# Kernel tuning notes

Measured on AMD Instinct MI355X. Metric: run time of the kernel, lower is better.

The kernel has to match this reference:

```python
import jax, jax.numpy as jnp
import numpy as np

N_USERS = 40000
N_POIS = 20000
D = 128
N_EDGES = 500000
N_LAYERS = 2
B = 256
NPOS = 100
TOPK = 20


def setup_inputs() -> dict:
    key = jax.random.key(0)
    ks = jax.random.split(key, 24)
    # guarantee every user row / poi col has at least one edge (avoids 0-norm rows)
    er = jnp.concatenate([jnp.arange(N_USERS, dtype=jnp.int32),
                          jax.random.randint(ks[0], (N_EDGES - N_USERS,), 0, N_USERS, jnp.int32)])
    ec = jnp.concatenate([jnp.arange(N_USERS, dtype=jnp.int32) % N_POIS,
                          jax.random.randint(ks[1], (N_EDGES - N_USERS,), 0, N_POIS, jnp.int32)])
    w0 = lambda k, shape: jax.random.normal(k, shape, jnp.float32) * 0.05
    return {
        'edge_row': er,
        'edge_col': ec,
        'click_vals': jax.random.uniform(ks[2], (N_EDGES,), jnp.float32),
        'favor_vals': jax.random.uniform(ks[3], (N_EDGES,), jnp.float32),
        'consume_vals': jax.random.uniform(ks[4], (N_EDGES,), jnp.float32),
        'uid_embed': w0(ks[5], (N_USERS, D)),
        'pid_embed': w0(ks[6], (N_POIS, D)),
        'user_index': jax.random.randint(ks[7], (B, 1), 0, N_USERS, jnp.int32),
        'poi_index': jax.random.randint(ks[8], (B, NPOS), 0, N_POIS, jnp.int32),
        'labels': (jax.random.uniform(ks[9], (B, NPOS)) < 0.5).astype(jnp.float32),
        'global_user_feature': w0(ks[10], (N_USERS, D)),
        'w': w0(ks[11], (1, 3)),
        'fw': w0(ks[12], (3, 1)),
        'W_user_click': w0(ks[13], (D, D)),
        'W_poi_click': w0(ks[14], (D, D)),
        'W_user_favor': w0(ks[15], (D, D)),
        'W_poi_favor': w0(ks[16], (D, D)),
        'W_user_consume': w0(ks[17], (D, D)),
        'W_poi_consume': w0(ks[18], (D, D)),
        'Ws': w0(ks[19], (D, D)),
        'bs_bias': w0(ks[20], (D,)),
    }


def reference(edge_row, edge_col, click_vals, favor_vals, consume_vals, uid_embed, pid_embed,
              user_index, poi_index, labels, global_user_feature, w, fw,
              W_user_click, W_poi_click, W_user_favor, W_poi_favor,
              W_user_consume, W_poi_consume, Ws, bs_bias):
    n_users, n_pois = uid_embed.shape[0], pid_embed.shape[0]
    batch_user = user_index.reshape(-1)

    def gcn(vals, Wu, Wp):
        # bipartite GCN propagation: A @ p (user side), A.T @ u (poi side)
        su, sp = uid_embed, pid_embed          # running sums of per-layer normalized features
        u, p = uid_embed, pid_embed            # un-normalized propagated features
        for _ in range(N_LAYERS):
            u = jax.ops.segment_sum(vals[:, None] * p[edge_col], edge_row, num_segments=n_users)
            su = su + u / jnp.linalg.norm(u, axis=1, keepdims=True)
            p = jax.ops.segment_sum(vals[:, None] * u[edge_row], edge_col, num_segments=n_pois)
            sp = sp + p / jnp.linalg.norm(p, axis=1, keepdims=True)
        uf = su @ Wu.T                         # final_user_linear (bias=False)
        pf = sp @ Wp.T                         # final_poi_linear (bias=False)
        return uf[batch_user] @ pf.T, uf       # [B, n_pois], [n_users, D]

    wn = jax.nn.softmax(w, axis=1)
    fwn = jax.nn.softmax(fw, axis=0)

    click_up, click_uf = gcn(click_vals, W_user_click, W_poi_click)
    favor_up, favor_uf = gcn(favor_vals + 1e-18 * click_vals, W_user_favor, W_poi_favor)
    consume_up, consume_uf = gcn(consume_vals + 1e-18 * click_vals, W_user_consume, W_poi_consume)

    alt = favor_up * wn[0, 0] + click_up * wn[0, 1] + consume_up * wn[0, 2]
    predict = jnp.take_along_axis(alt, poi_index, axis=1)                      # [B, NPOS]
    # BCEWithLogitsLoss (mean reduction), numerically stable form
    select_loss = jnp.mean(jax.nn.relu(predict) - predict * labels + jnp.log1p(jnp.exp(-jnp.abs(predict))))

    L = user_index.shape[1]
    cur = batch_user[jnp.arange(0, user_index.shape[0] * L, L)]                # first user of each row
    # gcn_user_feature stacked (favor, consume, click) @ fw
    id_feat = favor_uf * fwn[0, 0] + consume_uf * fwn[1, 0] + click_uf * fwn[2, 0]

    # Select_Layer (all inputs to matmuls are detached in the original)
    id_d = jax.lax.stop_gradient(id_feat)
    bs = id_d[cur] @ Ws.T + bs_bias
    uu = bs @ id_d.T                                                           # [B, n_users]
    top_score, top_idx = jax.lax.top_k(uu, TOPK)
    top_score = jax.nn.softmax(jax.lax.stop_gradient(top_score), axis=-1)
    neigh = jax.lax.stop_gradient(global_user_feature[top_idx])                # [B, TOPK, D]
    user_feature = jnp.einsum('bk,bkd->bd', top_score, neigh)
    return select_loss, user_feature
```

## Files before the change

### kernel.cpp

```cpp
#include <hip/hip_runtime.h>

#define N_USERS 40000
#define N_POIS  20000
#define DIM     128
#define N_EDGES 500000
#define BATCH   256
#define NPOS    100
#define TOPK    20
#define NCHUNK  128
#define CPT     313
#define SCHUNK  1024
#define RCH     40
#define CCH     20
#define LOSS_BLOCKS 25

typedef _Float16 f16x8 __attribute__((ext_vector_type(8)));
typedef float f32x4 __attribute__((ext_vector_type(4)));

__device__ __forceinline__ int iclamp(int x, int lo, int hi) {
    return x < lo ? lo : (x > hi ? hi : x);
}
__device__ __forceinline__ float2 h2f2(unsigned int u) {
    union { unsigned int u32; _Float16 h[2]; } v; v.u32 = u;
    return make_float2((float)v.h[0], (float)v.h[1]);
// ... 205 lines not shown
__global__ __launch_bounds__(256) void spmm_kernel(
        const int* __restrict__ ptr, const int4* __restrict__ pack,
        const unsigned short* __restrict__ src,
        unsigned short* __restrict__ raw_h,
        const float* __restrict__ base,
        float* __restrict__ acc, int nrows) {
    int wid = (blockIdx.x * blockDim.x + threadIdx.x) >> 6;
    int lane = threadIdx.x & 63;
    if (wid >= nrows) return;
    int beg = __builtin_amdgcn_readfirstlane(iclamp(ptr[wid], 0, N_EDGES));
    int end = __builtin_amdgcn_readfirstlane(iclamp(ptr[wid + 1], 0, N_EDGES));
    if (end < beg) end = beg;
    float ax = 0.f, ay = 0.f;
    int e = beg;
    int lo2 = lane * 2;
    for (; e + 8 <= end; e += 8) {
        int4 q0 = pack[e + 0], q1 = pack[e + 1], q2 = pack[e + 2], q3 = pack[e + 3];
        int4 q4 = pack[e + 4], q5 = pack[e + 5], q6 = pack[e + 6], q7 = pack[e + 7];
        float v0 = pickvT<CH>(q0), v1 = pickvT<CH>(q1), v2 = pickvT<CH>(q2), v3 = pickvT<CH>(q3);
        float v4 = pickvT<CH>(q4), v5 = pickvT<CH>(q5), v6 = pickvT<CH>(q6), v7 = pickvT<CH>(q7);
        float2 p0 = h2f2(*(const unsigned int*)(src + (size_t)q0.x * DIM + lo2));
        float2 p1 = h2f2(*(const unsigned int*)(src + (size_t)q1.x * DIM + lo2));
        float2 p2 = h2f2(*(const unsigned int*)(src + (size_t)q2.x * DIM + lo2));
        float2 p3 = h2f2(*(const unsigned int*)(src + (size_t)q3.x * DIM + lo2));
        float2 p4 = h2f2(*(const unsigned int*)(src + (size_t)q4.x * DIM + lo2));
        float2 p5 = h2f2(*(const unsigned int*)(src + (size_t)q5.x * DIM + lo2));
        float2 p6 = h2f2(*(const unsigned int*)(src + (size_t)q6.x * DIM + lo2));
        float2 p7 = h2f2(*(const unsigned int*)(src + (size_t)q7.x * DIM + lo2));
        ax = fmaf(v0, p0.x, fmaf(v1, p1.x, fmaf(v2, p2.x, fmaf(v3, p3.x, ax))));
        ax = fmaf(v4, p4.x, fmaf(v5, p5.x, fmaf(v6, p6.x, fmaf(v7, p7.x, ax))));
        ay = fmaf(v0, p0.y, fmaf(v1, p1.y, fmaf(v2, p2.y, fmaf(v3, p3.y, ay))));
        ay = fmaf(v4, p4.y, fmaf(v5, p5.y, fmaf(v6, p6.y, fmaf(v7, p7.y, ay))));
    }
    if (e < end) {
        int last = end - 1;
        int e1 = e + 1 <= last ? e + 1 : last;
        int e2 = e + 2 <= last ? e + 2 : last;
        int e3 = e + 3 <= last ? e + 3 : last;
        int e4 = e + 4 <= last ? e + 4 : last;
        int e5 = e + 5 <= last ? e + 5 : last;
        int e6 = e + 6 <= last ? e + 6 : last;
        int e7 = e + 7 <= last ? e + 7 : last;
        int4 q0 = pack[e], q1 = pack[e1], q2 = pack[e2], q3 = pack[e3];
        int4 q4 = pack[e4], q5 = pack[e5], q6 = pack[e6], q7 = pack[e7];
        float v0 = pickvT<CH>(q0);
        float v1 = (e + 1 < end) ? pickvT<CH>(q1) : 0.f;
        float v2 = (e + 2 < end) ? pickvT<CH>(q2) : 0.f;
        float v3 = (e + 3 < end) ? pickvT<CH>(q3) : 0.f;
        float v4 = (e + 4 < end) ? pickvT<CH>(q4) : 0.f;
        float v5 = (e + 5 < end) ? pickvT<CH>(q5) : 0.f;
        float v6 = (e + 6 < end) ? pickvT<CH>(q6) : 0.f;
        float v7 = (e + 7 < end) ? pickvT<CH>(q7) : 0.f;
        float2 p0 = h2f2(*(const unsigned int*)(src + (size_t)q0.x * DIM + lo2));
        float2 p1 = h2f2(*(const unsigned int*)(src + (size_t)q1.x * DIM + lo2));
        float2 p2 = h2f2(*(const unsigned int*)(src + (size_t)q2.x * DIM + lo2));
        float2 p3 = h2f2(*(const unsigned int*)(src + (size_t)q3.x * DIM + lo2));
        float2 p4 = h2f2(*(const unsigned int*)(src + (size_t)q4.x * DIM + lo2));
        float2 p5 = h2f2(*(const unsigned int*)(src + (size_t)q5.x * DIM + lo2));
        float2 p6 = h2f2(*(const unsigned int*)(src + (size_t)q6.x * DIM + lo2));
        float2 p7 = h2f2(*(const unsigned int*)(src + (size_t)q7.x * DIM + lo2));
        ax = fmaf(v0, p0.x, fmaf(v1, p1.x, fmaf(v2, p2.x, fmaf(v3, p3.x, ax))));
        ax = fmaf(v4, p4.x, fmaf(v5, p5.x, fmaf(v6, p6.x, fmaf(v7, p7.x, ax))));
        ay = fmaf(v0, p0.y, fmaf(v1, p1.y, fmaf(v2, p2.y, fmaf(v3, p3.y, ay))));
        ay = fmaf(v4, p4.y, fmaf(v5, p5.y, fmaf(v6, p6.y, fmaf(v7, p7.y, ay))));
    }
    float n2 = ax * ax + ay * ay;
    #pragma unroll
    for (int o = 32; o > 0; o >>= 1) n2 += __shfl_xor(n2, o, 64);
    float inv = rsqrtf(fmaxf(n2, 1e-30f));
    *(unsigned int*)(raw_h + (size_t)wid * DIM + lo2) = f2h2(ax, ay);
    float2 bv = *(const float2*)(base + (size_t)wid * DIM + lo2);
    *(float2*)(acc + (size_t)wid * DIM + lo2) =
        make_float2(bv.x + ax * inv, bv.y + ay * inv);
}

__global__ __launch_bounds__(256) void spmm3_kernel(
        const int* __restrict__ ptr, const int4* __restrict__ pack,
        const unsigned short* __restrict__ src,
        unsigned short* __restrict__ r0, unsigned short* __restrict__ r1,
        unsigned short* __restrict__ r2, int nrows) {
    int wid = (blockIdx.x * blockDim.x + threadIdx.x) >> 6;
    int lane = threadIdx.x & 63;
    if (wid >= nrows) return;
    int beg = __builtin_amdgcn_readfirstlane(iclamp(ptr[wid], 0, N_EDGES));
    int end = __builtin_amdgcn_readfirstlane(iclamp(ptr[wid + 1], 0, N_EDGES));
    if (end < beg) end = beg;
    float a0x = 0.f, a0y = 0.f, a1x = 0.f, a1y = 0.f, a2x = 0.f, a2y = 0.f;
    int e = beg;
    int lo2 = lane * 2;
    for (; e + 4 <= end; e += 4) {
        int4 q0 = pack[e + 0], q1 = pack[e + 1], q2 = pack[e + 2], q3 = pack[e + 3];
        float2 p0 = h2f2(*(const unsigned int*)(src + (size_t)q0.x * DIM + lo2));
        float2 p1 = h2f2(*(const unsigned int*)(src + (size_t)q1.x * DIM + lo2));
        float2 p2 = h2f2(*(const unsigned int*)(src + (size_t)q2.x * DIM + lo2));
        float2 p3 = h2f2(*(const unsigned int*)(src + (size_t)q3.x * DIM + lo2));
        a0x = fmaf(__int_as_float(q0.y), p0.x, fmaf(__int_as_float(q1.y), p1.x,
              fmaf(__int_as_float(q2.y), p2.x, fmaf(__int_as_float(q3.y), p3.x, a0x))));
// ... 244 lines not shown
    float k0 = x0.x * x0.x + x0.y * x0.y;
    float k1 = x1.x * x1.x + x1.y * x1.y;
    float k2 = x2.x * x2.x + x2.y * x2.y;
    #pragma unroll
    for (int oo = 32; oo > 0; oo >>= 1) {
        m0 += __shfl_xor(m0, oo, 64); m1 += __shfl_xor(m1, oo, 64); m2 += __shfl_xor(m2, oo, 64);
        k0 += __shfl_xor(k0, oo, 64); k1 += __shfl_xor(k1, oo, 64); k2 += __shfl_xor(k2, oo, 64);
    }
    float im0 = rsqrtf(fmaxf(m0, 1e-30f)), ik0 = rsqrtf(fmaxf(k0, 1e-30f));
    float im1 = rsqrtf(fmaxf(m1, 1e-30f)), ik1 = rsqrtf(fmaxf(k1, 1e-30f));
    float im2 = rsqrtf(fmaxf(m2, 1e-30f)), ik2 = rsqrtf(fmaxf(k2, 1e-30f));
    float2 bv = *(const float2*)(pid + o);
    *(float2*)(sp0 + o) = make_float2(bv.x + x0.x * ik0 + a0x * im0, bv.y + x0.y * ik0 + a0y * im0);
    *(float2*)(sp1 + o) = make_float2(bv.x + x1.x * ik1 + a1x * im1, bv.y + x1.y * ik1 + a1y * im1);
    *(float2*)(sp2 + o) = make_float2(bv.x + x2.x * ik2 + a2x * im2, bv.y + x2.y * ik2 + a2y * im2);
}

template<int CH>
__global__ __launch_bounds__(256) void spmm_l2u_kernel(
        const int* __restrict__ ptr, const int4* __restrict__ pack,
        const unsigned short* __restrict__ src,
        unsigned short* __restrict__ u1raw,
        const float* __restrict__ uid,
        float* __restrict__ su, int nrows) {
    int wid = (blockIdx.x * blockDim.x + threadIdx.x) >> 6;
    int lane = threadIdx.x & 63;
    if (wid >= nrows) return;
    int beg = __builtin_amdgcn_readfirstlane(iclamp(ptr[wid], 0, N_EDGES));
    int end = __builtin_amdgcn_readfirstlane(iclamp(ptr[wid + 1], 0, N_EDGES));
    if (end < beg) end = beg;
    float ax = 0.f, ay = 0.f;
    int e = beg;
    int lo2 = lane * 2;
    for (; e + 8 <= end; e += 8) {
        int4 q0 = pack[e + 0], q1 = pack[e + 1], q2 = pack[e + 2], q3 = pack[e + 3];
        int4 q4 = pack[e + 4], q5 = pack[e + 5], q6 = pack[e + 6], q7 = pack[e + 7];
        float v0 = pickvT<CH>(q0), v1 = pickvT<CH>(q1), v2 = pickvT<CH>(q2), v3 = pickvT<CH>(q3);
        float v4 = pickvT<CH>(q4), v5 = pickvT<CH>(q5), v6 = pickvT<CH>(q6), v7 = pickvT<CH>(q7);
        float2 p0 = h2f2(*(const unsigned int*)(src + (size_t)q0.x * DIM + lo2));
        float2 p1 = h2f2(*(const unsigned int*)(src + (size_t)q1.x * DIM + lo2));
        float2 p2 = h2f2(*(const unsigned int*)(src + (size_t)q2.x * DIM + lo2));
        float2 p3 = h2f2(*(const unsigned int*)(src + (size_t)q3.x * DIM + lo2));
        float2 p4 = h2f2(*(const unsigned int*)(src + (size_t)q4.x * DIM + lo2));
        float2 p5 = h2f2(*(const unsigned int*)(src + (size_t)q5.x * DIM + lo2));
        float2 p6 = h2f2(*(const unsigned int*)(src + (size_t)q6.x * DIM + lo2));
        float2 p7 = h2f2(*(const unsigned int*)(src + (size_t)q7.x * DIM + lo2));
        ax = fmaf(v0, p0.x, fmaf(v1, p1.x, fmaf(v2, p2.x, fmaf(v3, p3.x, ax))));
        ax = fmaf(v4, p4.x, fmaf(v5, p5.x, fmaf(v6, p6.x, fmaf(v7, p7.x, ax))));
        ay = fmaf(v0, p0.y, fmaf(v1, p1.y, fmaf(v2, p2.y, fmaf(v3, p3.y, ay))));
        ay = fmaf(v4, p4.y, fmaf(v5, p5.y, fmaf(v6, p6.y, fmaf(v7, p7.y, ay))));
    }
    if (e < end) {
        int last = end - 1;
        int e1 = e + 1 <= last ? e + 1 : last;
        int e2 = e + 2 <= last ? e + 2 : last;
        int e3 = e + 3 <= last ? e + 3 : last;
        int e4 = e + 4 <= last ? e + 4 : last;
        int e5 = e + 5 <= last ? e + 5 : last;
        int e6 = e + 6 <= last ? e + 6 : last;
        int e7 = e + 7 <= last ? e + 7 : last;
        int4 q0 = pack[e], q1 = pack[e1], q2 = pack[e2], q3 = pack[e3];
        int4 q4 = pack[e4], q5 = pack[e5], q6 = pack[e6], q7 = pack[e7];
        float v0 = pickvT<CH>(q0);
        float v1 = (e + 1 < end) ? pickvT<CH>(q1) : 0.f;
        float v2 = (e + 2 < end) ? pickvT<CH>(q2) : 0.f;
        float v3 = (e + 3 < end) ? pickvT<CH>(q3) : 0.f;
        float v4 = (e + 4 < end) ? pickvT<CH>(q4) : 0.f;
        float v5 = (e + 5 < end) ? pickvT<CH>(q5) : 0.f;
        float v6 = (e + 6 < end) ? pickvT<CH>(q6) : 0.f;
        float v7 = (e + 7 < end) ? pickvT<CH>(q7) : 0.f;
        float2 p0 = h2f2(*(const unsigned int*)(src + (size_t)q0.x * DIM + lo2));
        float2 p1 = h2f2(*(const unsigned int*)(src + (size_t)q1.x * DIM + lo2));
        float2 p2 = h2f2(*(const unsigned int*)(src + (size_t)q2.x * DIM + lo2));
        float2 p3 = h2f2(*(const unsigned int*)(src + (size_t)q3.x * DIM + lo2));
        float2 p4 = h2f2(*(const unsigned int*)(src + (size_t)q4.x * DIM + lo2));
        float2 p5 = h2f2(*(const unsigned int*)(src + (size_t)q5.x * DIM + lo2));
        float2 p6 = h2f2(*(const unsigned int*)(src + (size_t)q6.x * DIM + lo2));
        float2 p7 = h2f2(*(const unsigned int*)(src + (size_t)q7.x * DIM + lo2));
        ax = fmaf(v0, p0.x, fmaf(v1, p1.x, fmaf(v2, p2.x, fmaf(v3, p3.x, ax))));
        ax = fmaf(v4, p4.x, fmaf(v5, p5.x, fmaf(v6, p6.x, fmaf(v7, p7.x, ax))));
        ay = fmaf(v0, p0.y, fmaf(v1, p1.y, fmaf(v2, p2.y, fmaf(v3, p3.y, ay))));
        ay = fmaf(v4, p4.y, fmaf(v5, p5.y, fmaf(v6, p6.y, fmaf(v7, p7.y, ay))));
    }
    size_t o = (size_t)wid * DIM + lo2;
    float2 u1 = h2f2(*(const unsigned int*)(u1raw + o));
    float n2a = ax * ax + ay * ay;
    float n2b = u1.x * u1.x + u1.y * u1.y;
    #pragma unroll
    for (int oo = 32; oo > 0; oo >>= 1) {
        n2a += __shfl_xor(n2a, oo, 64);
        n2b += __shfl_xor(n2b, oo, 64);
    }
    float i2 = rsqrtf(fmaxf(n2a, 1e-30f));
    float i1 = rsqrtf(fmaxf(n2b, 1e-30f));
    *(unsigned int*)(u1raw + o) = f2h2(ax, ay);
    float2 bv = *(const float2*)(uid + o);
    *(float2*)(su + o) = make_float2(bv.x + u1.x * i1 + ax * i2,
                                     bv.y + u1.y * i1 + ay * i2);
}

template<int CH>
__global__ __launch_bounds__(256) void spmm_l2p_kernel(
        const int* __restrict__ ptr, const int4* __restrict__ pack,
        const unsigned short* __restrict__ src,
        const unsigned short* __restrict__ p1raw,
        const float* __restrict__ pid,
        float* __restrict__ sp, int nrows) {
    int wid = (blockIdx.x * blockDim.x + threadIdx.x) >> 6;
    int lane = threadIdx.x & 63;
    if (wid >= nrows) return;
    int beg = __builtin_amdgcn_readfirstlane(iclamp(ptr[wid], 0, N_EDGES));
    int end = __builtin_amdgcn_readfirstlane(iclamp(ptr[wid + 1], 0, N_EDGES));
    if (end < beg) end = beg;
    float ax = 0.f, ay = 0.f;
    int e = beg;
    int lo2 = lane * 2;
    for (; e + 8 <= end; e += 8) {
        int4 q0 = pack[e + 0], q1 = pack[e + 1], q2 = pack[e + 2], q3 = pack[e + 3];
        int4 q4 = pack[e + 4], q5 = pack[e + 5], q6 = pack[e + 6], q7 = pack[e + 7];
        float v0 = pickvT<CH>(q0), v1 = pickvT<CH>(q1), v2 = pickvT<CH>(q2), v3 = pickvT<CH>(q3);
        float v4 = pickvT<CH>(q4), v5 = pickvT<CH>(q5), v6 = pickvT<CH>(q6), v7 = pickvT<CH>(q7);
        float2 p0 = h2f2(*(const unsigned int*)(src + (size_t)q0.x * DIM + lo2));
        float2 p1 = h2f2(*(const unsigned int*)(src + (size_t)q1.x * DIM + lo2));
        float2 p2 = h2f2(*(const unsigned int*)(src + (size_t)q2.x * DIM + lo2));
        float2 p3 = h2f2(*(const unsigned int*)(src + (size_t)q3.x * DIM + lo2));
        float2 p4 = h2f2(*(const unsigned int*)(src + (size_t)q4.x * DIM + lo2));
        float2 p5 = h2f2(*(const unsigned int*)(src + (size_t)q5.x * DIM + lo2));
        float2 p6 = h2f2(*(const unsigned int*)(src + (size_t)q6.x * DIM + lo2));
        float2 p7 = h2f2(*(const unsigned int*)(src + (size_t)q7.x * DIM + lo2));
        ax = fmaf(v0, p0.x, fmaf(v1, p1.x, fmaf(v2, p2.x, fmaf(v3, p3.x, ax))));
        ax = fmaf(v4, p4.x, fmaf(v5, p5.x, fmaf(v6, p6.x, fmaf(v7, p7.x, ax))));
        ay = fmaf(v0, p0.y, fmaf(v1, p1.y, fmaf(v2, p2.y, fmaf(v3, p3.y, ay))));
        ay = fmaf(v4, p4.y, fmaf(v5, p5.y, fmaf(v6, p6.y, fmaf(v7, p7.y, ay))));
    }
    if (e < end) {
        int last = end - 1;
        int e1 = e + 1 <= last ? e + 1 : last;
        int e2 = e + 2 <= last ? e + 2 : last;
        int e3 = e + 3 <= last ? e + 3 : last;
        int e4 = e + 4 <= last ? e + 4 : last;
        int e5 = e + 5 <= last ? e + 5 : last;
        int e6 = e + 6 <= last ? e + 6 : last;
        int e7 = e + 7 <= last ? e + 7 : last;
        int4 q0 = pack[e], q1 = pack[e1], q2 = pack[e2], q3 = pack[e3];
        int4 q4 = pack[e4], q5 = pack[e5], q6 = pack[e6], q7 = pack[e7];
        float v0 = pickvT<CH>(q0);
        float v1 = (e + 1 < end) ? pickvT<CH>(q1) : 0.f;
        float v2 = (e + 2 < end) ? pickvT<CH>(q2) : 0.f;
        float v3 = (e + 3 < end) ? pickvT<CH>(q3) : 0.f;
        float v4 = (e + 4 < end) ? pickvT<CH>(q4) : 0.f;
        float v5 = (e + 5 < end) ? pickvT<CH>(q5) : 0.f;
        float v6 = (e + 6 < end) ? pickvT<CH>(q6) : 0.f;
        float v7 = (e + 7 < end) ? pickvT<CH>(q7) : 0.f;
        float2 p0 = h2f2(*(const unsigned int*)(src + (size_t)q0.x * DIM + lo2));
        float2 p1 = h2f2(*(const unsigned int*)(src + (size_t)q1.x * DIM + lo2));
        float2 p2 = h2f2(*(const unsigned int*)(src + (size_t)q2.x * DIM + lo2));
        float2 p3 = h2f2(*(const unsigned int*)(src + (size_t)q3.x * DIM + lo2));
        float2 p4 = h2f2(*(const unsigned int*)(src + (size_t)q4.x * DIM + lo2));
        float2 p5 = h2f2(*(const unsigned int*)(src + (size_t)q5.x * DIM + lo2));
        float2 p6 = h2f2(*(const unsigned int*)(src + (size_t)q6.x * DIM + lo2));
        float2 p7 = h2f2(*(const unsigned int*)(src + (size_t)q7.x * DIM + lo2));
        ax = fmaf(v0, p0.x, fmaf(v1, p1.x, fmaf(v2, p2.x, fmaf(v3, p3.x, ax))));
        ax = fmaf(v4, p4.x, fmaf(v5, p5.x, fmaf(v6, p6.x, fmaf(v7, p7.x, ax))));
        ay = fmaf(v0, p0.y, fmaf(v1, p1.y, fmaf(v2, p2.y, fmaf(v3, p3.y, ay))));
        ay = fmaf(v4, p4.y, fmaf(v5, p5.y, fmaf(v6, p6.y, fmaf(v7, p7.y, ay))));
    }
    size_t o = (size_t)wid * DIM + lo2;
    float2 p1v = h2f2(*(const unsigned int*)(p1raw + o));
    float n2a = ax * ax + ay * ay;
    float n2b = p1v.x * p1v.x + p1v.y * p1v.y;
    #pragma unroll
    for (int oo = 32; oo > 0; oo >>= 1) {
        n2a += __shfl_xor(n2a, oo, 64);
        n2b += __shfl_xor(n2b, oo, 64);
    }
    float i2 = rsqrtf(fmaxf(n2a, 1e-30f));
    float i1 = rsqrtf(fmaxf(n2b, 1e-30f));
    float2 bv = *(const float2*)(pid + o);
    *(float2*)(sp + o) = make_float2(bv.x + p1v.x * i1 + ax * i2,
                                     bv.y + p1v.y * i1 + ay * i2);
}

__global__ __launch_bounds__(256) void gemm_mfma_kernel(
        const float* __restrict__ A, const float* __restrict__ W,
        float* __restrict__ store, float* __restrict__ accum,
        _Float16* __restrict__ accum_h,
        const float* __restrict__ fw3, int fsel, int first, int M) {
    int w = threadIdx.x >> 6, l = threadIdx.x & 63;
    int lg = l >> 4, lc = l & 15;
    int j0 = w * 32;
    float coef = accum ? softmax3(fw3, fsel) : 0.f;
    f16x8 Bf[2][4];
    #pragma unroll
    for (int t = 0; t < 2; t++) {
        const float* wr = W + (size_t)(j0 + t * 16 + lc) * DIM + lg * 8;
        #pragma unroll
        for (int s = 0; s < 4; s++) Bf[t][s] = frag8(wr + s * 32);
    }
// ... 7 lines not shown
        #pragma unroll
        for (int s = 0; s < 4; s++) Af[s] = frag8(arow + s * 32);
        f32x4 acc0 = {0.f, 0.f, 0.f, 0.f};
        f32x4 acc1 = {0.f, 0.f, 0.f, 0.f};
        #pragma unroll
        for (int s = 0; s < 4; s++) {
            acc0 = __builtin_amdgcn_mfma_f32_16x16x32_f16(Af[s], Bf[0][s], acc0, 0, 0, 0);
            acc1 = __builtin_amdgcn_mfma_f32_16x16x32_f16(Af[s], Bf[1][s], acc1, 0, 0, 0);
        }
        int rbase = u0 + lg * 4;
        #pragma unroll
        for (int r = 0; r < 4; r++) {
            int row = rbase + r;
            if (row >= M) continue;
            size_t o0 = (size_t)row * DIM + j0 + lc;
            size_t o1 = o0 + 16;
            if (store) { store[o0] = acc0[r]; store[o1] = acc1[r]; }
            if (accum) {
                float p0 = first ? 0.f : accum[o0];
                float p1 = first ? 0.f : accum[o1];
                float n0 = p0 + coef * acc0[r];
                float n1 = p1 + coef * acc1[r];
                accum[o0] = n0;
                accum[o1] = n1;
                if (accum_h) {
                    accum_h[o0] = (_Float16)n0;
                    accum_h[o1] = (_Float16)n1;
                }
            }
        }
    }
}

__global__ void ufsel_kernel(const float* __restrict__ su, const float* __restrict__ W,
                             const int* __restrict__ uidx, float* __restrict__ outsel) {
    int b = blockIdx.x, j = threadIdx.x;
    __shared__ float ar[128];
    int u = iclamp(uidx[b], 0, N_USERS - 1);
    ar[j] = su[(size_t)u * DIM + j];
    __syncthreads();
    const float4* Wr = (const float4*)(W + (size_t)j * DIM);
    float acc = 0.f;
    #pragma unroll 8
    for (int q = 0; q < 32; q++) {
        float4 wq = Wr[q];
        acc = fmaf(ar[4 * q + 0], wq.x, acc);
        acc = fmaf(ar[4 * q + 1], wq.y, acc);
        acc = fmaf(ar[4 * q + 2], wq.z, acc);
        acc = fmaf(ar[4 * q + 3], wq.w, acc);
    }
    outsel[(size_t)b * DIM + j] = acc;
}

__global__ __launch_bounds__(256) void predict_kernel(
        const float* __restrict__ ufs, const float* __restrict__ pf,
        const int* __restrict__ pidx, const float* __restrict__ w3,
        int wsel, int first, float* __restrict__ alt) {
    int wid = (blockIdx.x * blockDim.x + threadIdx.x) >> 6;
    int lane = threadIdx.x & 63;
    if (wid >= BATCH * NPOS) return;
    int b = wid / NPOS;
    int poi = iclamp(pidx[wid], 0, N_POIS - 1);
    const float2 uv = *(const float2*)(ufs + (size_t)b * DIM + lane * 2);
    const float2 pv = *(const float2*)(pf + (size_t)poi * DIM + lane * 2);
    float s = uv.x * pv.x + uv.y * pv.y;
    #pragma unroll
    for (int o = 32; o > 0; o >>= 1) s += __shfl_xor(s, o, 64);
    if (lane == 0) {
        float coef = softmax3(w3, wsel);
        float prev = first ? 0.f : alt[wid];
        alt[wid] = prev + coef * s;
    }
}

__global__ void loss_part_kernel(const float* __restrict__ alt, const float* __restrict__ labels,
                                 float* __restrict__ part) {
    int b = blockIdx.x, t = threadIdx.x;
    int i = b * 1024 + t * 4;
    float4 x4 = *(const float4*)(alt + i);
    float4 y4 = *(const float4*)(labels + i);
    float s = 0.f;
    s += fmaxf(x4.x, 0.f) - x4.x * y4.x + log1pf(expf(-fabsf(x4.x)));
    s += fmaxf(x4.y, 0.f) - x4.y * y4.y + log1pf(expf(-fabsf(x4.y)));
    s += fmaxf(x4.z, 0.f) - x4.z * y4.z + log1pf(expf(-fabsf(x4.z)));
// ... 227 lines not shown
    int* rcnt = cnts;
    int* ccnt = cnts + N_USERS;
    int* scanws = (int*)carve(4 * 2 * (RCH + CCH) + 4 * 64);
    int* rsum = scanws;
    int* csum = rsum + RCH;
    int* rbase = csum + CCH;
    int* cbase = rbase + RCH;
    float* losspart = (float*)carve(4 * (LOSS_BLOCKS + 7));
    int4* rpack = (int4*)carve(16ll * N_EDGES);
    int4* cpack = (int4*)carve(16ll * N_EDGES);
    unsigned short* pid_h = (unsigned short*)carve(2ll * N_POIS * DIM);
    unsigned short* utr0 = (unsigned short*)carve(2ll * N_USERS * DIM);
    unsigned short* ptr_h = (unsigned short*)carve(2ll * N_POIS * DIM);
    float* su  = (float*)carve(4ll * N_USERS * DIM);
    float* sp  = (float*)carve(4ll * N_POIS * DIM);
    float* idf = (float*)carve(4ll * N_USERS * DIM);
    float* pf = (float*)utr0;
    float* cand_s = su;
    int*   cand_i = (int*)(su + (size_t)NCHUNK * BATCH * TOPK);
    _Float16* idf_h = (_Float16*)rpack;
    _Float16* bst_h = (_Float16*)bst;
    int* rord = (int*)su;
    int* cord = rord + N_EDGES;
    unsigned short* utr1 = (unsigned short*)carve(2ll * N_USERS * DIM);
    unsigned short* utr2 = (unsigned short*)carve(2ll * N_USERS * DIM);
    unsigned short* p1b1 = (unsigned short*)carve(2ll * N_POIS * DIM);
    unsigned short* p1b2 = (unsigned short*)carve(2ll * N_POIS * DIM);
    bool fused = (off <= ws_size);
    float* su1 = (float*)carve(4ll * N_USERS * DIM);
    float* su2 = (float*)carve(4ll * N_USERS * DIM);
    float* sp1 = (float*)carve(4ll * N_POIS * DIM);
    float* sp2 = (float*)carve(4ll * N_POIS * DIM);
    bool fused2 = (off <= ws_size);

    zero_kernel<<<(N_USERS + N_POIS + 255) / 256, 256, 0, stream>>>(
        (unsigned int*)cnts, N_USERS + N_POIS);
    cast_f16_kernel<<<(N_POIS * DIM / 2 + 255) / 256, 256, 0, stream>>>(pid, pid_h, N_POIS * DIM / 2);
    hist_kernel<<<(N_EDGES / 4 + 255) / 256, 256, 0, stream>>>(er, ec, rcnt, ccnt, rord, cord);
    dim3 sg2(RCH, 2);
    chunksum_kernel<<<sg2, 256, 0, stream>>>(rcnt, ccnt, rsum, csum);
    chunkscan_kernel<<<1, 128, 0, stream>>>(rsum, csum, rbase, cbase, rptr, cptr);
    scatterscan_kernel<<<sg2, 256, 0, stream>>>(rcnt, ccnt, rbase, cbase, rptr, cptr);
    fill_kernel<<<(N_EDGES / 4 + 255) / 256, 256, 0, stream>>>(
        er, ec, rptr, cptr, rord, cord, rpack, cpack, click, favor, consume);

    struct Ch { const float* Wu; const float* Wp; int wsel; int fsel; };
    Ch chs[3] = { { Wuc,  Wpc,  1, 2 },
                  { Wufv, Wpfv, 0, 0 },
                  { Wuco, Wpco, 2, 1 } };

    const int UGB = N_USERS / 64;
    const int PGB = (N_POIS + 63) / 64;
    const int PW = N_POIS * 64 / 256;
    const int UW = N_USERS * 64 / 256;

    auto launch_spmm_poi = [&](int c, const unsigned short* src, unsigned short* raw,
                               const float* base, float* acc) {
        if (c == 0)      spmm_kernel<0><<<PW, 256, 0, stream>>>(cptr, cpack, src, raw, base, acc, N_POIS);
        else if (c == 1) spmm_kernel<1><<<PW, 256, 0, stream>>>(cptr, cpack, src, raw, base, acc, N_POIS);
        else             spmm_kernel<2><<<PW, 256, 0, stream>>>(cptr, cpack, src, raw, base, acc, N_POIS);
    };
    auto launch_spmm_usr = [&](int c, const unsigned short* src, unsigned short* raw,
                               const float* base, float* acc) {
        if (c == 0)      spmm_kernel<0><<<UW, 256, 0, stream>>>(rptr, rpack, src, raw, base, acc, N_USERS);
        else if (c == 1) spmm_kernel<1><<<UW, 256, 0, stream>>>(rptr, rpack, src, raw, base, acc, N_USERS);
        else             spmm_kernel<2><<<UW, 256, 0, stream>>>(rptr, rpack, src, raw, base, acc, N_USERS);
    };
    auto launch_l2u = [&](int c, const unsigned short* src, unsigned short* u1raw) {
        if (c == 0)      spmm_l2u_kernel<0><<<UW, 256, 0, stream>>>(rptr, rpack, src, u1raw, uid, su, N_USERS);
        else if (c == 1) spmm_l2u_kernel<1><<<UW, 256, 0, stream>>>(rptr, rpack, src, u1raw, uid, su, N_USERS);
        else             spmm_l2u_kernel<2><<<UW, 256, 0, stream>>>(rptr, rpack, src, u1raw, uid, su, N_USERS);
    };
    auto launch_l2p = [&](int c, const unsigned short* src, const unsigned short* p1raw) {
        if (c == 0)      spmm_l2p_kernel<0><<<PW, 256, 0, stream>>>(cptr, cpack, src, p1raw, pid, sp, N_POIS);
        else if (c == 1) spmm_l2p_kernel<1><<<PW, 256, 0, stream>>>(cptr, cpack, src, p1raw, pid, sp, N_POIS);
        else             spmm_l2p_kernel<2><<<PW, 256, 0, stream>>>(cptr, cpack, src, p1raw, pid, sp, N_POIS);
    };

    if (fused2) {
        spmm3_kernel<<<UW, 256, 0, stream>>>(rptr, rpack, pid_h, utr0, utr1, utr2, N_USERS);
        spmm3p_kernel<<<PW, 256, 0, stream>>>(cptr, cpack, utr0, utr1, utr2,
                                              ptr_h, p1b1, p1b2, N_POIS);
        spmm_l2u3_kernel<<<UW, 256, 0, stream>>>(rptr, rpack, ptr_h, p1b1, p1b2,
                                                 utr0, utr1, utr2, uid, su, su1, su2, N_USERS);
        spmm_l2p3_kernel<<<PW, 256, 0, stream>>>(cptr, cpack, utr0, utr1, utr2,
                                                 ptr_h, p1b1, p1b2, pid, sp, sp1, sp2, N_POIS);
        float* sus[3] = { su, su1, su2 };
        float* sps[3] = { sp, sp1, sp2 };
        for (int c = 0; c < 3; c++) {
            gemm_mfma_kernel<<<UGB, 256, 0, stream>>>(
                sus[c], chs[c].Wu, nullptr, idf, (c == 2) ? idf_h : nullptr,
                fw3, chs[c].fsel, (c == 0) ? 1 : 0, N_USERS);
            ufsel_kernel<<<BATCH, 128, 0, stream>>>(sus[c], chs[c].Wu, uidx, ufs + (size_t)c * BATCH * DIM);
            gemm_mfma_kernel<<<PGB, 256, 0, stream>>>(
                sps[c], chs[c].Wp, pf, nullptr, nullptr, fw3, 0, 0, N_POIS);
            predict_kernel<<<BATCH * NPOS * 64 / 256, 256, 0, stream>>>(
                ufs + (size_t)c * BATCH * DIM, pf, pidx, w3, chs[c].wsel, (c == 0) ? 1 : 0, alt);
        }
    } else if (fused) {
        spmm3_kernel<<<UW, 256, 0, stream>>>(rptr, rpack, pid_h, utr0, utr1, utr2, N_USERS);
        spmm3p_kernel<<<PW, 256, 0, stream>>>(cptr, cpack, utr0, utr1, utr2,
                                              ptr_h, p1b1, p1b2, N_POIS);
        unsigned short* p1b[3] = { ptr_h, p1b1, p1b2 };
        unsigned short* utr[3] = { utr0, utr1, utr2 };
        for (int c = 0; c < 3; c++) {
            launch_l2u(c, p1b[c], utr[c]);
            launch_l2p(c, utr[c], p1b[c]);
            gemm_mfma_kernel<<<UGB, 256, 0, stream>>>(
                su, chs[c].Wu, nullptr, idf, (c == 2) ? idf_h : nullptr,
                fw3, chs[c].fsel, (c == 0) ? 1 : 0, N_USERS);
            ufsel_kernel<<<BATCH, 128, 0, stream>>>(su, chs[c].Wu, uidx, ufs + (size_t)c * BATCH * DIM);
            gemm_mfma_kernel<<<PGB, 256, 0, stream>>>(
                sp, chs[c].Wp, pf, nullptr, nullptr, fw3, 0, 0, N_POIS);
            predict_kernel<<<BATCH * NPOS * 64 / 256, 256, 0, stream>>>(
                ufs + (size_t)c * BATCH * DIM, pf, pidx, w3, chs[c].wsel, (c == 0) ? 1 : 0, alt);
        }
    } else {
        for (int c = 0; c < 3; c++) {
            launch_spmm_usr(c, pid_h, utr0, uid, su);
            launch_spmm_poi(c, utr0, ptr_h, pid, sp);
            launch_spmm_usr(c, ptr_h, utr0, su, su);
            launch_spmm_poi(c, utr0, ptr_h, sp, sp);
            gemm_mfma_kernel<<<UGB, 256, 0, stream>>>(
                su, chs[c].Wu, nullptr, idf, (c == 2) ? idf_h : nullptr,
                fw3, chs[c].fsel, (c == 0) ? 1 : 0, N_USERS);
            ufsel_kernel<<<BATCH, 128, 0, stream>>>(su, chs[c].Wu, uidx, ufs + (size_t)c * BATCH * DIM);
            gemm_mfma_kernel<<<PGB, 256, 0, stream>>>(
                sp, chs[c].Wp, pf, nullptr, nullptr, fw3, 0, 0, N_POIS);
            predict_kernel<<<BATCH * NPOS * 64 / 256, 256, 0, stream>>>(
                ufs + (size_t)c * BATCH * DIM, pf, pidx, w3, chs[c].wsel, (c == 0) ? 1 : 0, alt);
        }
// ... 10 lines not shown
```

Baseline: 626.3 us.

## Fuse per-channel GEMM/predict launches into batched three-channel kernels

The post-SpMM stage in the fused2 path used to run a loop of 12 launches (user GEMM, ufsel, poi GEMM, predict per channel). It now runs four kernels: one user GEMM that computes all three channels and applies the softmax weights in registers, one grid-y-batched poi GEMM writing three separate outputs into reused utr buffers, a batched ufsel, and one predict kernel that combines all channels. This removes launch overhead and the read-modify-write accumulation passes over idf and alt. Separately, the 8-way unrolled edge loops in several templated SpMM kernels are replaced with simple scalar loops, which may reduce memory-level parallelism in those kernels, though they appear to belong to the non-default paths.

Measured after the change: 569.7 us. -9.0%, faster.

```diff
diff --git a/kernel.cpp b/kernel.cpp
--- a/kernel.cpp
+++ b/kernel.cpp
@@ -261,37 +261,12 @@
         ay = fmaf(v0, p0.y, fmaf(v1, p1.y, fmaf(v2, p2.y, fmaf(v3, p3.y, ay))));
         ay = fmaf(v4, p4.y, fmaf(v5, p5.y, fmaf(v6, p6.y, fmaf(v7, p7.y, ay))));
     }
-    if (e < end) {
-        int last = end - 1;
-        int e1 = e + 1 <= last ? e + 1 : last;
-        int e2 = e + 2 <= last ? e + 2 : last;
-        int e3 = e + 3 <= last ? e + 3 : last;
-        int e4 = e + 4 <= last ? e + 4 : last;
-        int e5 = e + 5 <= last ? e + 5 : last;
-        int e6 = e + 6 <= last ? e + 6 : last;
-        int e7 = e + 7 <= last ? e + 7 : last;
-        int4 q0 = pack[e], q1 = pack[e1], q2 = pack[e2], q3 = pack[e3];
-        int4 q4 = pack[e4], q5 = pack[e5], q6 = pack[e6], q7 = pack[e7];
-        float v0 = pickvT<CH>(q0);
-        float v1 = (e + 1 < end) ? pickvT<CH>(q1) : 0.f;
-        float v2 = (e + 2 < end) ? pickvT<CH>(q2) : 0.f;
-        float v3 = (e + 3 < end) ? pickvT<CH>(q3) : 0.f;
-        float v4 = (e + 4 < end) ? pickvT<CH>(q4) : 0.f;
-        float v5 = (e + 5 < end) ? pickvT<CH>(q5) : 0.f;
-        float v6 = (e + 6 < end) ? pickvT<CH>(q6) : 0.f;
-        float v7 = (e + 7 < end) ? pickvT<CH>(q7) : 0.f;
-        float2 p0 = h2f2(*(const unsigned int*)(src + (size_t)q0.x * DIM + lo2));
-        float2 p1 = h2f2(*(const unsigned int*)(src + (size_t)q1.x * DIM + lo2));
-        float2 p2 = h2f2(*(const unsigned int*)(src + (size_t)q2.x * DIM + lo2));
-        float2 p3 = h2f2(*(const unsigned int*)(src + (size_t)q3.x * DIM + lo2));
-        float2 p4 = h2f2(*(const unsigned int*)(src + (size_t)q4.x * DIM + lo2));
-        float2 p5 = h2f2(*(const unsigned int*)(src + (size_t)q5.x * DIM + lo2));
-        float2 p6 = h2f2(*(const unsigned int*)(src + (size_t)q6.x * DIM + lo2));
-        float2 p7 = h2f2(*(const unsigned int*)(src + (size_t)q7.x * DIM + lo2));
-        ax = fmaf(v0, p0.x, fmaf(v1, p1.x, fmaf(v2, p2.x, fmaf(v3, p3.x, ax))));
-        ax = fmaf(v4, p4.x, fmaf(v5, p5.x, fmaf(v6, p6.x, fmaf(v7, p7.x, ax))));
-        ay = fmaf(v0, p0.y, fmaf(v1, p1.y, fmaf(v2, p2.y, fmaf(v3, p3.y, ay))));
-        ay = fmaf(v4, p4.y, fmaf(v5, p5.y, fmaf(v6, p6.y, fmaf(v7, p7.y, ay))));
+    for (; e < end; e++) {
+        int4 q = pack[e];
+        float v = pickvT<CH>(q);
+        float2 p = h2f2(*(const unsigned int*)(src + (size_t)q.x * DIM + lo2));
+        ax = fmaf(v, p.x, ax);
+        ay = fmaf(v, p.y, ay);
     }
     float n2 = ax * ax + ay * ay;
     #pragma unroll
@@ -602,55 +577,12 @@
     float ax = 0.f, ay = 0.f;
     int e = beg;
     int lo2 = lane * 2;
-    for (; e + 8 <= end; e += 8) {
-        int4 q0 = pack[e + 0], q1 = pack[e + 1], q2 = pack[e + 2], q3 = pack[e + 3];
-        int4 q4 = pack[e + 4], q5 = pack[e + 5], q6 = pack[e + 6], q7 = pack[e + 7];
-        float v0 = pickvT<CH>(q0), v1 = pickvT<CH>(q1), v2 = pickvT<CH>(q2), v3 = pickvT<CH>(q3);
-        float v4 = pickvT<CH>(q4), v5 = pickvT<CH>(q5), v6 = pickvT<CH>(q6), v7 = pickvT<CH>(q7);
-        float2 p0 = h2f2(*(const unsigned int*)(src + (size_t)q0.x * DIM + lo2));
-        float2 p1 = h2f2(*(const unsigned int*)(src + (size_t)q1.x * DIM + lo2));
-        float2 p2 = h2f2(*(const unsigned int*)(src + (size_t)q2.x * DIM + lo2));
-        float2 p3 = h2f2(*(const unsigned int*)(src + (size_t)q3.x * DIM + lo2));
-        float2 p4 = h2f2(*(const unsigned int*)(src + (size_t)q4.x * DIM + lo2));
-        float2 p5 = h2f2(*(const unsigned int*)(src + (size_t)q5.x * DIM + lo2));
-        float2 p6 = h2f2(*(const unsigned int*)(src + (size_t)q6.x * DIM + lo2));
-        float2 p7 = h2f2(*(const unsigned int*)(src + (size_t)q7.x * DIM + lo2));
-        ax = fmaf(v0, p0.x, fmaf(v1, p1.x, fmaf(v2, p2.x, fmaf(v3, p3.x, ax))));
-        ax = fmaf(v4, p4.x, fmaf(v5, p5.x, fmaf(v6, p6.x, fmaf(v7, p7.x, ax))));
-        ay = fmaf(v0, p0.y, fmaf(v1, p1.y, fmaf(v2, p2.y, fmaf(v3, p3.y, ay))));
-        ay = fmaf(v4, p4.y, fmaf(v5, p5.y, fmaf(v6, p6.y, fmaf(v7, p7.y, ay))));
-    }
-    if (e < end) {
-        int last = end - 1;
-        int e1 = e + 1 <= last ? e + 1 : last;
-        int e2 = e + 2 <= last ? e + 2 : last;
-        int e3 = e + 3 <= last ? e + 3 : last;
-        int e4 = e + 4 <= last ? e + 4 : last;
-        int e5 = e + 5 <= last ? e + 5 : last;
-        int e6 = e + 6 <= last ? e + 6 : last;
-        int e7 = e + 7 <= last ? e + 7 : last;
-        int4 q0 = pack[e], q1 = pack[e1], q2 = pack[e2], q3 = pack[e3];
-        int4 q4 = pack[e4], q5 = pack[e5], q6 = pack[e6], q7 = pack[e7];
-        float v0 = pickvT<CH>(q0);
-        float v1 = (e + 1 < end) ? pickvT<CH>(q1) : 0.f;
-        float v2 = (e + 2 < end) ? pickvT<CH>(q2) : 0.f;
-        float v3 = (e + 3 < end) ? pickvT<CH>(q3) : 0.f;
-        float v4 = (e + 4 < end) ? pickvT<CH>(q4) : 0.f;
-        float v5 = (e + 5 < end) ? pickvT<CH>(q5) : 0.f;
-        float v6 = (e + 6 < end) ? pickvT<CH>(q6) : 0.f;
-        float v7 = (e + 7 < end) ? pickvT<CH>(q7) : 0.f;
-        float2 p0 = h2f2(*(const unsigned int*)(src + (size_t)q0.x * DIM + lo2));
-        float2 p1 = h2f2(*(const unsigned int*)(src + (size_t)q1.x * DIM + lo2));
-        float2 p2 = h2f2(*(const unsigned int*)(src + (size_t)q2.x * DIM + lo2));
-        float2 p3 = h2f2(*(const unsigned int*)(src + (size_t)q3.x * DIM + lo2));
-        float2 p4 = h2f2(*(const unsigned int*)(src + (size_t)q4.x * DIM + lo2));
-        float2 p5 = h2f2(*(const unsigned int*)(src + (size_t)q5.x * DIM + lo2));
-        float2 p6 = h2f2(*(const unsigned int*)(src + (size_t)q6.x * DIM + lo2));
-        float2 p7 = h2f2(*(const unsigned int*)(src + (size_t)q7.x * DIM + lo2));
-        ax = fmaf(v0, p0.x, fmaf(v1, p1.x, fmaf(v2, p2.x, fmaf(v3, p3.x, ax))));
-        ax = fmaf(v4, p4.x, fmaf(v5, p5.x, fmaf(v6, p6.x, fmaf(v7, p7.x, ax))));
-        ay = fmaf(v0, p0.y, fmaf(v1, p1.y, fmaf(v2, p2.y, fmaf(v3, p3.y, ay))));
-        ay = fmaf(v4, p4.y, fmaf(v5, p5.y, fmaf(v6, p6.y, fmaf(v7, p7.y, ay))));
+    for (; e < end; e++) {
+        int4 q = pack[e];
+        float v = pickvT<CH>(q);
+        float2 p = h2f2(*(const unsigned int*)(src + (size_t)q.x * DIM + lo2));
+        ax = fmaf(v, p.x, ax);
+        ay = fmaf(v, p.y, ay);
     }
     size_t o = (size_t)wid * DIM + lo2;
     float2 u1 = h2f2(*(const unsigned int*)(u1raw + o));
@@ -685,55 +617,12 @@
     float ax = 0.f, ay = 0.f;
     int e = beg;
     int lo2 = lane * 2;
-    for (; e + 8 <= end; e += 8) {
-        int4 q0 = pack[e + 0], q1 = pack[e + 1], q2 = pack[e + 2], q3 = pack[e + 3];
-        int4 q4 = pack[e + 4], q5 = pack[e + 5], q6 = pack[e + 6], q7 = pack[e + 7];
-        float v0 = pickvT<CH>(q0), v1 = pickvT<CH>(q1), v2 = pickvT<CH>(q2), v3 = pickvT<CH>(q3);
-        float v4 = pickvT<CH>(q4), v5 = pickvT<CH>(q5), v6 = pickvT<CH>(q6), v7 = pickvT<CH>(q7);
-        float2 p0 = h2f2(*(const unsigned int*)(src + (size_t)q0.x * DIM + lo2));
-        float2 p1 = h2f2(*(const unsigned int*)(src + (size_t)q1.x * DIM + lo2));
-        float2 p2 = h2f2(*(const unsigned int*)(src + (size_t)q2.x * DIM + lo2));
-        float2 p3 = h2f2(*(const unsigned int*)(src + (size_t)q3.x * DIM + lo2));
-        float2 p4 = h2f2(*(const unsigned int*)(src + (size_t)q4.x * DIM + lo2));
-        float2 p5 = h2f2(*(const unsigned int*)(src + (size_t)q5.x * DIM + lo2));
-        float2 p6 = h2f2(*(const unsigned int*)(src + (size_t)q6.x * DIM + lo2));
-        float2 p7 = h2f2(*(const unsigned int*)(src + (size_t)q7.x * DIM + lo2));
-        ax = fmaf(v0, p0.x, fmaf(v1, p1.x, fmaf(v2, p2.x, fmaf(v3, p3.x, ax))));
-        ax = fmaf(v4, p4.x, fmaf(v5, p5.x, fmaf(v6, p6.x, fmaf(v7, p7.x, ax))));
-        ay = fmaf(v0, p0.y, fmaf(v1, p1.y, fmaf(v2, p2.y, fmaf(v3, p3.y, ay))));
-        ay = fmaf(v4, p4.y, fmaf(v5, p5.y, fmaf(v6, p6.y, fmaf(v7, p7.y, ay))));
-    }
-    if (e < end) {
-        int last = end - 1;
-        int e1 = e + 1 <= last ? e + 1 : last;
-        int e2 = e + 2 <= last ? e + 2 : last;
-        int e3 = e + 3 <= last ? e + 3 : last;
-        int e4 = e + 4 <= last ? e + 4 : last;
-        int e5 = e + 5 <= last ? e + 5 : last;
-        int e6 = e + 6 <= last ? e + 6 : last;
-        int e7 = e + 7 <= last ? e + 7 : last;
-        int4 q0 = pack[e], q1 = pack[e1], q2 = pack[e2], q3 = pack[e3];
-        int4 q4 = pack[e4], q5 = pack[e5], q6 = pack[e6], q7 = pack[e7];
-        float v0 = pickvT<CH>(q0);
-        float v1 = (e + 1 < end) ? pickvT<CH>(q1) : 0.f;
-        float v2 = (e + 2 < end) ? pickvT<CH>(q2) : 0.f;
-        float v3 = (e + 3 < end) ? pickvT<CH>(q3) : 0.f;
-        float v4 = (e + 4 < end) ? pickvT<CH>(q4) : 0.f;
-        float v5 = (e + 5 < end) ? pickvT<CH>(q5) : 0.f;
-        float v6 = (e + 6 < end) ? pickvT<CH>(q6) : 0.f;
-        float v7 = (e + 7 < end) ? pickvT<CH>(q7) : 0.f;
-        float2 p0 = h2f2(*(const unsigned int*)(src + (size_t)q0.x * DIM + lo2));
-        float2 p1 = h2f2(*(const unsigned int*)(src + (size_t)q1.x * DIM + lo2));
-        float2 p2 = h2f2(*(const unsigned int*)(src + (size_t)q2.x * DIM + lo2));
-        float2 p3 = h2f2(*(const unsigned int*)(src + (size_t)q3.x * DIM + lo2));
-        float2 p4 = h2f2(*(const unsigned int*)(src + (size_t)q4.x * DIM + lo2));
-        float2 p5 = h2f2(*(const unsigned int*)(src + (size_t)q5.x * DIM + lo2));
-        float2 p6 = h2f2(*(const unsigned int*)(src + (size_t)q6.x * DIM + lo2));
-        float2 p7 = h2f2(*(const unsigned int*)(src + (size_t)q7.x * DIM + lo2));
-        ax = fmaf(v0, p0.x, fmaf(v1, p1.x, fmaf(v2, p2.x, fmaf(v3, p3.x, ax))));
-        ax = fmaf(v4, p4.x, fmaf(v5, p5.x, fmaf(v6, p6.x, fmaf(v7, p7.x, ax))));
-        ay = fmaf(v0, p0.y, fmaf(v1, p1.y, fmaf(v2, p2.y, fmaf(v3, p3.y, ay))));
-        ay = fmaf(v4, p4.y, fmaf(v5, p5.y, fmaf(v6, p6.y, fmaf(v7, p7.y, ay))));
+    for (; e < end; e++) {
+        int4 q = pack[e];
+        float v = pickvT<CH>(q);
+        float2 p = h2f2(*(const unsigned int*)(src + (size_t)q.x * DIM + lo2));
+        ax = fmaf(v, p.x, ax);
+        ay = fmaf(v, p.y, ay);
     }
     size_t o = (size_t)wid * DIM + lo2;
     float2 p1v = h2f2(*(const unsigned int*)(p1raw + o));
@@ -807,6 +696,169 @@
     }
 }
 
+__global__ __launch_bounds__(256) void gemm_mfma3u_kernel(
+        const float* __restrict__ A0, const float* __restrict__ A1, const float* __restrict__ A2,
+        const float* __restrict__ W0, const float* __restrict__ W1, const float* __restrict__ W2,
+        float* __restrict__ idf, _Float16* __restrict__ idf_h,
+        const float* __restrict__ fw3, int M) {
+    int w = threadIdx.x >> 6, l = threadIdx.x & 63;
+    int lg = l >> 4, lc = l & 15;
+    int j0 = w * 32;
+    float cf0 = softmax3(fw3, 2);
+    float cf1 = softmax3(fw3, 0);
+    float cf2 = softmax3(fw3, 1);
+    f16x8 B0[2][4], B1[2][4], B2[2][4];
+    #pragma unroll
+    for (int t = 0; t < 2; t++) {
+        size_t ro = (size_t)(j0 + t * 16 + lc) * DIM + lg * 8;
+        const float* wr0 = W0 + ro;
+        const float* wr1 = W1 + ro;
+        const float* wr2 = W2 + ro;
+        #pragma unroll
+        for (int s = 0; s < 4; s++) {
+            B0[t][s] = frag8(wr0 + s * 32);
+            B1[t][s] = frag8(wr1 + s * 32);
+            B2[t][s] = frag8(wr2 + s * 32);
+        }
+    }
+    int base = blockIdx.x * 64;
+    #pragma unroll
+    for (int rt = 0; rt < 4; rt++) {
+        int u0 = base + rt * 16;
+        int ar = u0 + lc; if (ar > M - 1) ar = M - 1;
+        size_t aro = (size_t)ar * DIM + lg * 8;
+        f32x4 f0 = {0.f, 0.f, 0.f, 0.f};
+        f32x4 f1 = {0.f, 0.f, 0.f, 0.f};
+        {
+            const float* arow = A0 + aro;
+            f16x8 Af[4];
+            #pragma unroll
+            for (int s = 0; s < 4; s++) Af[s] = frag8(arow + s * 32);
+            f32x4 a0 = {0.f, 0.f, 0.f, 0.f};
+            f32x4 a1 = {0.f, 0.f, 0.f, 0.f};
+            #pragma unroll
+            for (int s = 0; s < 4; s++) {
+                a0 = __builtin_amdgcn_mfma_f32_16x16x32_f16(Af[s], B0[0][s], a0, 0, 0, 0);
+                a1 = __builtin_amdgcn_mfma_f32_16x16x32_f16(Af[s], B0[1][s], a1, 0, 0, 0);
+            }
+            f0 += a0 * cf0; f1 += a1 * cf0;
+        }
+        {
+            const float* arow = A1 + aro;
+            f16x8 Af[4];
+            #pragma unroll
+            for (int s = 0; s < 4; s++) Af[s] = frag8(arow + s * 32);
+            f32x4 a0 = {0.f, 0.f, 0.f, 0.f};
+            f32x4 a1 = {0.f, 0.f, 0.f, 0.f};
+            #pragma unroll
+            for (int s = 0; s < 4; s++) {
+                a0 = __builtin_amdgcn_mfma_f32_16x16x32_f16(Af[s], B1[0][s], a0, 0, 0, 0);
+                a1 = __builtin_amdgcn_mfma_f32_16x16x32_f16(Af[s], B1[1][s], a1, 0, 0, 0);
+            }
+            f0 += a0 * cf1; f1 += a1 * cf1;
+        }
+        {
+            const float* arow = A2 + aro;
+            f16x8 Af[4];
+            #pragma unroll
+            for (int s = 0; s < 4; s++) Af[s] = frag8(arow + s * 32);
+            f32x4 a0 = {0.f, 0.f, 0.f, 0.f};
+            f32x4 a1 = {0.f, 0.f, 0.f, 0.f};
+            #pragma unroll
+            for (int s = 0; s < 4; s++) {
+                a0 = __builtin_amdgcn_mfma_f32_16x16x32_f16(Af[s], B2[0][s], a0, 0, 0, 0);
+                a1 = __builtin_amdgcn_mfma_f32_16x16x32_f16(Af[s], B2[1][s], a1, 0, 0, 0);
+            }
+            f0 += a0 * cf2; f1 += a1 * cf2;
+        }
+        int rbase = u0 + lg * 4;
+        #pragma unroll
+        for (int r = 0; r < 4; r++) {
+            int row = rbase + r;
+            if (row >= M) continue;
+            size_t o0 = (size_t)row * DIM + j0 + lc;
+            size_t o1 = o0 + 16;
+            idf[o0] = f0[r];
+            idf[o1] = f1[r];
+            idf_h[o0] = (_Float16)f0[r];
+            idf_h[o1] = (_Float16)f1[r];
+        }
+    }
+}
+
+__global__ __launch_bounds__(256) void gemm_poi3_kernel(
+        const float* __restrict__ S0, const float* __restrict__ S1, const float* __restrict__ S2,
+        const float* __restrict__ Wp0, const float* __restrict__ Wp1, const float* __restrict__ Wp2,
+        float* __restrict__ P0, float* __restrict__ P1, float* __restrict__ P2, int M) {
+    int c = blockIdx.y;
+    const float* A = (c == 0) ? S0 : ((c == 1) ? S1 : S2);
+    const float* W = (c == 0) ? Wp0 : ((c == 1) ? Wp1 : Wp2);
+    float* P = (c == 0) ? P0 : ((c == 1) ? P1 : P2);
+    int w = threadIdx.x >> 6, l = threadIdx.x & 63;
+    int lg = l >> 4, lc = l & 15;
+    int j0 = w * 32;
+    f16x8 Bf[2][4];
+    #pragma unroll
+    for (int t = 0; t < 2; t++) {
+        const float* wr = W + (size_t)(j0 + t * 16 + lc) * DIM + lg * 8;
+        #pragma unroll
+        for (int s = 0; s < 4; s++) Bf[t][s] = frag8(wr + s * 32);
+    }
+    int base = blockIdx.x * 64;
+    #pragma unroll
+    for (int rt = 0; rt < 4; rt++) {
+        int u0 = base + rt * 16;
+        int ar = u0 + lc; if (ar > M - 1) ar = M - 1;
+        const float* arow = A + (size_t)ar * DIM + lg * 8;
+        f16x8 Af[4];
+        #pragma unroll
+        for (int s = 0; s < 4; s++) Af[s] = frag8(arow + s * 32);
+        f32x4 acc0 = {0.f, 0.f, 0.f, 0.f};
+        f32x4 acc1 = {0.f, 0.f, 0.f, 0.f};
+        #pragma unroll
+        for (int s = 0; s < 4; s++) {
+            acc0 = __builtin_amdgcn_mfma_f32_16x16x32_f16(Af[s], Bf[0][s], acc0, 0, 0, 0);
+            acc1 = __builtin_amdgcn_mfma_f32_16x16x32_f16(Af[s], Bf[1][s], acc1, 0, 0, 0);
+        }
+        int rbase = u0 + lg * 4;
+        #pragma unroll
+        for (int r = 0; r < 4; r++) {
+            int row = rbase + r;
+            if (row >= M) continue;
+            size_t o0 = (size_t)row * DIM + j0 + lc;
+            size_t o1 = o0 + 16;
+            P[o0] = acc0[r];
+            P[o1] = acc1[r];
+        }
+    }
+}
+
+__global__ void ufsel3_kernel(const float* __restrict__ S0, const float* __restrict__ S1,
+                              const float* __restrict__ S2,
+                              const float* __restrict__ Wu0, const float* __restrict__ Wu1,
+                              const float* __restrict__ Wu2,
+                              const int* __restrict__ uidx, float* __restrict__ ufs) {
+    int b = blockIdx.x, j = threadIdx.x;
+    int c = blockIdx.y;
+    const float* su_c = (c == 0) ? S0 : ((c == 1) ? S1 : S2);
+    const float* W = (c == 0) ? Wu0 : ((c == 1) ? Wu1 : Wu2);
+    __shared__ float ar[128];
+    int u = iclamp(uidx[b], 0, N_USERS - 1);
+    ar[j] = su_c[(size_t)u * DIM + j];
+    __syncthreads();
+    const float4* Wr = (const float4*)(W + (size_t)j * DIM);
+    float acc = 0.f;
+    #pragma unroll 8
+    for (int q = 0; q < 32; q++) {
+        float4 wq = Wr[q];
+        acc = fmaf(ar[4 * q + 0], wq.x, acc);
+        acc = fmaf(ar[4 * q + 1], wq.y, acc);
+        acc = fmaf(ar[4 * q + 2], wq.z, acc);
+        acc = fmaf(ar[4 * q + 3], wq.w, acc);
+    }
+    ufs[(size_t)c * BATCH * DIM + (size_t)b * DIM + j] = acc;
+}
+
 __global__ void ufsel_kernel(const float* __restrict__ su, const float* __restrict__ W,
                              const int* __restrict__ uidx, float* __restrict__ outsel) {
     int b = blockIdx.x, j = threadIdx.x;
@@ -825,6 +877,35 @@
         acc = fmaf(ar[4 * q + 3], wq.w, acc);
     }
     outsel[(size_t)b * DIM + j] = acc;
+}
+
+__global__ __launch_bounds__(256) void predict3_kernel(
+        const float* __restrict__ ufs,
+        const float* __restrict__ pf0, const float* __restrict__ pf1, const float* __restrict__ pf2,
+        const int* __restrict__ pidx, const float* __restrict__ w3,
+        float* __restrict__ alt) {
+    int wid = (blockIdx.x * blockDim.x + threadIdx.x) >> 6;
+    int lane = threadIdx.x & 63;
+    if (wid >= BATCH * NPOS) return;
+    int b = wid / NPOS;
+    int poi = iclamp(pidx[wid], 0, N_POIS - 1);
+    float cc0 = softmax3(w3, 1);
+    float cc1 = softmax3(w3, 0);
+    float cc2 = softmax3(w3, 2);
+    size_t ub = (size_t)b * DIM + lane * 2;
+    size_t pb = (size_t)poi * DIM + lane * 2;
+    float2 u0 = *(const float2*)(ufs + 0 * BATCH * DIM + ub);
+    float2 u1 = *(const float2*)(ufs + 1 * BATCH * DIM + ub);
+    float2 u2 = *(const float2*)(ufs + 2 * BATCH * DIM + ub);
+    float2 p0 = *(const float2*)(pf0 + pb);
+    float2 p1 = *(const float2*)(pf1 + pb);
+    float2 p2 = *(const float2*)(pf2 + pb);
+    float s = cc0 * (u0.x * p0.x + u0.y * p0.y)
+            + cc1 * (u1.x * p1.x + u1.y * p1.y)
+            + cc2 * (u2.x * p2.x + u2.y * p2.y);
+    #pragma unroll
+    for (int o = 32; o > 0; o >>= 1) s += __shfl_xor(s, o, 64);
+    if (lane == 0) alt[wid] = s;
 }
 
 __global__ __launch_bounds__(256) void predict_kernel(
@@ -1118,6 +1199,9 @@
     float* sp1 = (float*)carve(4ll * N_POIS * DIM);
     float* sp2 = (float*)carve(4ll * N_POIS * DIM);
     bool fused2 = (off <= ws_size);
+    float* pf0 = (float*)utr0;
+    float* pf1 = (float*)utr1;
+    float* pf2 = (float*)utr2;
 
     zero_kernel<<<(N_USERS + N_POIS + 255) / 256, 256, 0, stream>>>(
         (unsigned int*)cnts, N_USERS + N_POIS);
@@ -1171,18 +1255,15 @@
                                                  utr0, utr1, utr2, uid, su, su1, su2, N_USERS);
         spmm_l2p3_kernel<<<PW, 256, 0, stream>>>(cptr, cpack, utr0, utr1, utr2,
                                                  ptr_h, p1b1, p1b2, pid, sp, sp1, sp2, N_POIS);
-        float* sus[3] = { su, su1, su2 };
-        float* sps[3] = { sp, sp1, sp2 };
-        for (int c = 0; c < 3; c++) {
-            gemm_mfma_kernel<<<UGB, 256, 0, stream>>>(
-                sus[c], chs[c].Wu, nullptr, idf, (c == 2) ? idf_h : nullptr,
-                fw3, chs[c].fsel, (c == 0) ? 1 : 0, N_USERS);
-            ufsel_kernel<<<BATCH, 128, 0, stream>>>(sus[c], chs[c].Wu, uidx, ufs + (size_t)c * BATCH * DIM);
-            gemm_mfma_kernel<<<PGB, 256, 0, stream>>>(
-                sps[c], chs[c].Wp, pf, nullptr, nullptr, fw3, 0, 0, N_POIS);
-            predict_kernel<<<BATCH * NPOS * 64 / 256, 256, 0, stream>>>(
-                ufs + (size_t)c * BATCH * DIM, pf, pidx, w3, chs[c].wsel, (c == 0) ? 1 : 0, alt);
-        }
+        gemm_mfma3u_kernel<<<UGB, 256, 0, stream>>>(
+            su, su1, su2, Wuc, Wufv, Wuco, idf, idf_h, fw3, N_USERS);
+        dim3 ug(BATCH, 3);
+        ufsel3_kernel<<<ug, 128, 0, stream>>>(su, su1, su2, Wuc, Wufv, Wuco, uidx, ufs);
+        dim3 pg(PGB, 3);
+        gemm_poi3_kernel<<<pg, 256, 0, stream>>>(sp, sp1, sp2, Wpc, Wpfv, Wpco,
+                                                 pf0, pf1, pf2, N_POIS);
+        predict3_kernel<<<BATCH * NPOS * 64 / 256, 256, 0, stream>>>(
+            ufs, pf0, pf1, pf2, pidx, w3, alt);
     } else if (fused) {
         spmm3_kernel<<<UW, 256, 0, stream>>>(rptr, rpack, pid_h, utr0, utr1, utr2, N_USERS);
         spmm3p_kernel<<<PW, 256, 0, stream>>>(cptr, cpack, utr0, utr1, utr2,
```
